# Kernel tuning notes

Hardware: AMD Instinct MI355X
Metric: run time of the kernel (lower is better)

The kernel has to match this reference:

```python
import jax, jax.numpy as jnp
import numpy as np

D = 512
H = 8
DH = D // H
EPS = 1e-5


def _layernorm(x, g, b):
    mu = jnp.mean(x, axis=-1, keepdims=True)
    var = jnp.mean((x - mu) ** 2, axis=-1, keepdims=True)
    return (x - mu) * jax.lax.rsqrt(var + EPS) * g + b


def setup_inputs() -> dict:
    key = jax.random.key(0)
    ks = jax.random.split(key, 10)
    B, S = 4, 2048
    s = 1.0 / np.sqrt(D)
    return {
        "x": jax.random.normal(ks[0], (B, S, D), dtype=jnp.float32),
        "Wq": jax.random.normal(ks[1], (D, D), dtype=jnp.float32) * s,
        "Wk": jax.random.normal(ks[2], (D, D), dtype=jnp.float32) * s,
        "Wv": jax.random.normal(ks[3], (D, D), dtype=jnp.float32) * s,
        "Wo": jax.random.normal(ks[4], (D, D), dtype=jnp.float32) * s,
        "W1": jax.random.normal(ks[5], (4 * D, D), dtype=jnp.float32) * s,
        "b1": jnp.zeros((4 * D,), dtype=jnp.float32),
        "W2": jax.random.normal(ks[6], (D, 4 * D), dtype=jnp.float32) * (1.0 / np.sqrt(4 * D)),
        "b2": jnp.zeros((D,), dtype=jnp.float32),
        "g1": jnp.ones((D,), dtype=jnp.float32),
        "bb1": jnp.zeros((D,), dtype=jnp.float32),
        "g2": jnp.ones((D,), dtype=jnp.float32),
        "bb2": jnp.zeros((D,), dtype=jnp.float32),
    }


def reference(x, Wq, Wk, Wv, Wo, W1, b1, W2, b2, g1, bb1, g2, bb2):
    B, S, _ = x.shape
    # projections (torch Linear: y = x @ W.T), split heads: chunk(-1) == reshape to [B,S,H,DH]
    q = (x @ Wq.T).reshape(B, S, H, DH).transpose(0, 2, 1, 3)  # [B,H,S,DH]
    k = (x @ Wk.T).reshape(B, S, H, DH).transpose(0, 2, 1, 3)
    v = (x @ Wv.T).reshape(B, S, H, DH).transpose(0, 2, 1, 3)
    scores = jnp.einsum("bhsd,bhtd->bhst", q, k) / np.sqrt(DH)  # [B,H,S,S]
    attn = jax.nn.softmax(scores, axis=-1)
    ctx = jnp.einsum("bhst,bhtd->bhsd", attn, v)  # [B,H,S,DH]
    ctx = ctx.transpose(0, 2, 1, 3).reshape(B, S, D)
    h = _layernorm(x + ctx @ Wo.T, g1, bb1)
    mlp = jax.nn.relu(h @ W1.T + b1) @ W2.T + b2
    return _layernorm(h + mlp, g2, bb2)
```

## Files before the change

### kernel.cpp

```cpp
#include <hip/hip_runtime.h>
#include <hip/hip_bf16.h>
#include <cstdint>
#include <cstddef>

typedef short bf16x8 __attribute__((ext_vector_type(8)));
typedef float floatx4 __attribute__((ext_vector_type(4)));
typedef unsigned int uintx4 __attribute__((ext_vector_type(4)));
typedef unsigned short u16;

constexpr int B = 4, S = 2048, D = 512, H = 8, DH = 64;
constexpr int M_ROWS = B * S;
constexpr int D4 = 4 * D;
constexpr float QSCALE = 0.18033688011112042f;

__device__ __forceinline__ u16 f2b(float f) {
  unsigned u = __builtin_bit_cast(unsigned, f);
  u += 0x7fff + ((u >> 16) & 1);
  return (u16)(u >> 16);
}

__device__ __forceinline__ bf16x8 ldfrag(const u16* p) {
  return *reinterpret_cast<const bf16x8*>(p);
}

__device__ __forceinline__ floatx4 mfma16(bf16x8 a, bf16x8 b, floatx4 c) {
  return __builtin_amdgcn_mfma_f32_16x16x32_bf16(a, b, c, 0, 0, 0);
}

__device__ __forceinline__ ushort4 f2b4(float4 v) {
  ushort4 r;
  r.x = f2b(v.x); r.y = f2b(v.y); r.z = f2b(v.z); r.w = f2b(v.w);
  return r;
}

__device__ __forceinline__ void gld16(const u16* g, u16* l) {
  __builtin_amdgcn_global_load_lds(
      (const __attribute__((address_space(1))) void*)g,
      (__attribute__((address_space(3))) void*)l, 16, 0, 0);
}

__global__ void cast_all_kernel(const float4* __restrict__ x,
                                const float4* __restrict__ w1, const float4* __restrict__ w2,
                                const float4* __restrict__ wq, const float4* __restrict__ wk,
                                const float4* __restrict__ wv, const float4* __restrict__ wo,
                                ushort4* __restrict__ xb,
                                ushort4* __restrict__ w1b, ushort4* __restrict__ w2b,
                                ushort4* __restrict__ wqb, ushort4* __restrict__ wkb,
                                ushort4* __restrict__ wvb, ushort4* __restrict__ wob) {
  int i = blockIdx.x * blockDim.x + threadIdx.x;
  constexpr int NX = (M_ROWS * D) / 4;
  constexpr int N1 = (D4 * D) / 4;
  constexpr int NS = (D * D) / 4;
  if (i < NX) { xb[i] = f2b4(x[i]); return; }
  i -= NX;
  if (i < N1) { w1b[i] = f2b4(w1[i]); return; }
  i -= N1;
  if (i < N1) { w2b[i] = f2b4(w2[i]); return; }
  i -= N1;
  const int sel = i >> 16, off = i & (NS - 1);
  const float4* src = sel == 0 ? wq : sel == 1 ? wk : sel == 2 ? wv : wo;
  ushort4* dst = sel == 0 ? wqb : sel == 1 ? wkb : sel == 2 ? wvb : wob;
  dst[off] = f2b4(src[off]);
}

template <int EPI>
__global__ __launch_bounds__(256) void gemm_bt(
    const u16* __restrict__ A, const u16* __restrict__ W,
    const float* __restrict__ bias, void* __restrict__ out0, void* __restrict__ out1,
    int M, int N, int K, int klen) {
  __shared__ __align__(16) u16 As[2][128 * 32];
  __shared__ __align__(16) u16 Bs[2][128 * 32];
  const int wave = threadIdx.x >> 6, lane = threadIdx.x & 63;
  const int quad = lane >> 4, l16 = lane & 15;
  const int rowB = blockIdx.y * 128, colB = blockIdx.x * 128;
  const int rowW = (wave >> 1) * 64, colW = (wave & 1) * 64;
  const int koff = blockIdx.z * klen;
  void* out = blockIdx.z ? out1 : out0;

  floatx4 acc[4][4];
#pragma unroll
  for (int i = 0; i < 4; i++)
#pragma unroll
    for (int j = 0; j < 4; j++) acc[i][j] = (floatx4){0.f,0.f,0.f,0.f};

  const u16* gA = A + (size_t)(rowB + wave * 32 + (lane >> 2)) * K + koff + (lane & 3) * 8;
  const u16* gB = W + (size_t)(colB + wave * 32 + (lane >> 2)) * K + koff + (lane & 3) * 8;
  const int lds_off = wave * 1024;

#pragma unroll
  for (int rr = 0; rr < 2; rr++) {
    gld16(gA + (size_t)rr * 16 * K, &As[0][lds_off + rr * 512]);
    gld16(gB + (size_t)rr * 16 * K, &Bs[0][lds_off + rr * 512]);
  }

  int buf = 0;
  for (int kc = 0; kc < klen; kc += 32, buf ^= 1) {
    __syncthreads();

    if (kc + 32 < klen) {
#pragma unroll
      for (int rr = 0; rr < 2; rr++) {
        gld16(gA + (size_t)rr * 16 * K + kc + 32, &As[buf ^ 1][lds_off + rr * 512]);
        gld16(gB + (size_t)rr * 16 * K + kc + 32, &Bs[buf ^ 1][lds_off + rr * 512]);
      }
    }

    bf16x8 a[4], b[4];
#pragma unroll
    for (int i = 0; i < 4; i++)
      a[i] = ldfrag(&As[buf][(rowW + i * 16 + l16) * 32 + quad * 8]);
#pragma unroll
    for (int j = 0; j < 4; j++)
      b[j] = ldfrag(&Bs[buf][(colW + j * 16 + l16) * 32 + quad * 8]);
#pragma unroll
    for (int i = 0; i < 4; i++)
#pragma unroll
      for (int j = 0; j < 4; j++) acc[i][j] = mfma16(a[i], b[j], acc[i][j]);
  }

#pragma unroll
  for (int i = 0; i < 4; i++) {
#pragma unroll
    for (int j = 0; j < 4; j++) {
      const int gn = colB + colW + j * 16 + l16;
      const float bv = (EPI == 1) ? bias[gn] : 0.f;
#pragma unroll
      for (int r = 0; r < 4; r++) {
        const int gm = rowB + rowW + i * 16 + quad * 4 + r;
        float v = acc[i][j][r] + bv;
        if (EPI == 0) {
          ((float*)out)[(size_t)gm * N + gn] = v;
        } else {
          v = v > 0.f ? v : 0.f;
          ((u16*)out)[(size_t)gm * N + gn] = f2b(v);
        }
      }
    }
  }
}

__global__ __launch_bounds__(256) void qkv_gemm(
    const u16* __restrict__ xb,
    const u16* __restrict__ wq, const u16* __restrict__ wk, const u16* __restrict__ wv,
    u16* __restrict__ q, u16* __restrict__ k, u16* __restrict__ vT) {
  __shared__ __align__(16) u16 As[2][128 * 32];
  __shared__ __align__(16) u16 Bs[2][128 * 32];
  const int which = blockIdx.z;
  const u16* __restrict__ W = which == 0 ? wq : (which == 1 ? wk : wv);
  const int wave = threadIdx.x >> 6, lane = threadIdx.x & 63;
  const int quad = lane >> 4, l16 = lane & 15;
  const int rowB = blockIdx.y * 128, colB = blockIdx.x * 128;
  const int rowW = (wave >> 1) * 64, colW = (wave & 1) * 64;

  floatx4 acc[4][4];
#pragma unroll
  for (int i = 0; i < 4; i++)
#pragma unroll
    for (int j = 0; j < 4; j++) acc[i][j] = (floatx4){0.f,0.f,0.f,0.f};

  const u16* gA = xb + (size_t)(rowB + wave * 32 + (lane >> 2)) * D + (lane & 3) * 8;
  const u16* gB = W + (size_t)(colB + wave * 32 + (lane >> 2)) * D + (lane & 3) * 8;
  const int lds_off = wave * 1024;

#pragma unroll
  for (int rr = 0; rr < 2; rr++) {
    gld16(gA + (size_t)rr * 16 * D, &As[0][lds_off + rr * 512]);
    gld16(gB + (size_t)rr * 16 * D, &Bs[0][lds_off + rr * 512]);
  }

  int buf = 0;
  for (int kc = 0; kc < D; kc += 32, buf ^= 1) {
    __syncthreads();

    if (kc + 32 < D) {
#pragma unroll
      for (int rr = 0; rr < 2; rr++) {
        gld16(gA + (size_t)rr * 16 * D + kc + 32, &As[buf ^ 1][lds_off + rr * 512]);
        gld16(gB + (size_t)rr * 16 * D + kc + 32, &Bs[buf ^ 1][lds_off + rr * 512]);
      }
    }

    bf16x8 a[4], b[4];
#pragma unroll
    for (int i = 0; i < 4; i++)
      a[i] = ldfrag(&As[buf][(rowW + i * 16 + l16) * 32 + quad * 8]);
#pragma unroll
    for (int j = 0; j < 4; j++)
      b[j] = ldfrag(&Bs[buf][(colW + j * 16 + l16) * 32 + quad * 8]);
#pragma unroll
    for (int i = 0; i < 4; i++)
#pragma unroll
      for (int j = 0; j < 4; j++) acc[i][j] = mfma16(a[i], b[j], acc[i][j]);
  }

  const float oscale = (which == 0) ? QSCALE : 1.0f;
  u16* dst01 = which == 0 ? q : k;
#pragma unroll
  for (int i = 0; i < 4; i++) {
#pragma unroll
    for (int j = 0; j < 4; j++) {
      const int gn = colB + colW + j * 16 + l16;
      const int h = gn >> 6, dh = gn & 63;
#pragma unroll
      for (int r = 0; r < 4; r++) {
        const int gm = rowB + rowW + i * 16 + quad * 4 + r;
        const int bb = gm >> 11, s = gm & 2047;
        const u16 val = f2b(acc[i][j][r] * oscale);
        if (which < 2) {
          dst01[((((size_t)bb * H + h) * S) + s) * DH + dh] = val;
        } else {
          const int sl = s & 63;
          const int sw = (s & ~63) | (sl & 35) | ((sl & 12) << 1) | ((sl & 16) >> 2);
          vT[((((size_t)bb * H + h) * DH) + dh) * S + sw] = val;
        }
      }
    }
  }
}

__global__ __launch_bounds__(512, 1) void attn_kernel(
    const u16* __restrict__ q, const u16* __restrict__ k,
    const u16* __restrict__ vT, u16* __restrict__ ctxb) {
  __shared__ __align__(16) u16 kvlds[2][2][2][2][64 * 32];
  __shared__ __align__(16) float ltb[2][4][64];
  const int wave = threadIdx.x >> 6, lane = threadIdx.x & 63;
  const int quad = lane >> 4, l16 = lane & 15;
  const int pair = wave >> 1, khalf = wave & 1;
  const int blk = (blockIdx.x & 7) * 32 + (blockIdx.x >> 3);
  const int w = blk * 4 + pair;
  const int bh = w >> 5, qt = w & 31;
  const int bb = bh >> 3, h = bh & 7;

  const u16* qp = q + ((size_t)bh * S + qt * 64 + l16) * DH + quad * 8;
  bf16x8 qf[4][2];
#pragma unroll
  for (int t = 0; t < 4; t++) {
    qf[t][0] = ldfrag(qp + (size_t)t * 16 * DH);
    qf[t][1] = ldfrag(qp + (size_t)t * 16 * DH + 32);
  }

  const int st = pair * 64 + lane;
  const int srow = st >> 2, sp = (st & 3) * 8;
  const u16* kS = k + (size_t)bh * S * DH + (size_t)(khalf * 1024 + srow) * DH + sp;
  const u16* vS = vT + (size_t)bh * DH * S + (size_t)srow * S + khalf * 1024 + sp;

  floatx4 o[4][4];
#pragma unroll
  for (int t = 0; t < 4; t++)
#pragma unroll
    for (int c = 0; c < 4; c++) o[t][c] = (floatx4){0.f,0.f,0.f,0.f};
  float lacc[4] = {0.f, 0.f, 0.f, 0.f};

  gld16(kS, &kvlds[0][khalf][0][0][pair * 512]);
  gld16(kS + 32, &kvlds[0][khalf][0][1][pair * 512]);
  gld16(vS, &kvlds[0][khalf][1][0][pair * 512]);
  gld16(vS + 32, &kvlds[0][khalf][1][1][pair * 512]);

  int buf = 0;
  for (int kt = 0; kt < S / 2; kt += 64, buf ^= 1) {
    __syncthreads();

    bf16x8 kf[8], vf[8];
#pragma unroll
    for (int i = 0; i < 4; i++) {
      kf[2 * i]     = ldfrag(&kvlds[buf][khalf][0][0][(i * 16 + l16) * 32 + quad * 8]);
      kf[2 * i + 1] = ldfrag(&kvlds[buf][khalf][0][1][(i * 16 + l16) * 32 + quad * 8]);
      vf[2 * i]     = ldfrag(&kvlds[buf][khalf][1][0][(i * 16 + l16) * 32 + quad * 8]);
      vf[2 * i + 1] = ldfrag(&kvlds[buf][khalf][1][1][(i * 16 + l16) * 32 + quad * 8]);
    }

    if (kt + 64 < S / 2) {
      const int nb = buf ^ 1;
      gld16(kS + (size_t)(kt + 64) * DH, &kvlds[nb][khalf][0][0][pair * 512]);
      gld16(kS + (size_t)(kt + 64) * DH + 32, &kvlds[nb][khalf][0][1][pair * 512]);
      gld16(vS + kt + 64, &kvlds[nb][khalf][1][0][pair * 512]);
      gld16(vS + kt + 96, &kvlds[nb][khalf][1][1][pair * 512]);
    }

#pragma unroll
    for (int t = 0; t < 4; t++) {
      floatx4 sc[4];
      __builtin_amdgcn_s_setprio(1);
#pragma unroll
      for (int i = 0; i < 4; i++) {
        floatx4 z = (floatx4){0.f,0.f,0.f,0.f};
        z = mfma16(kf[2 * i], qf[t][0], z);
        z = mfma16(kf[2 * i + 1], qf[t][1], z);
        sc[i] = z;
      }
      __builtin_amdgcn_s_setprio(0);

      unsigned wd[8];
      float a = 0.f;
#pragma unroll
      for (int i = 0; i < 4; i++) {
        const float p0 = __builtin_amdgcn_exp2f(sc[i][0]);
        const float p1 = __builtin_amdgcn_exp2f(sc[i][1]);
        const float p2 = __builtin_amdgcn_exp2f(sc[i][2]);
        const float p3 = __builtin_amdgcn_exp2f(sc[i][3]);
        a += (p0 + p1) + (p2 + p3);
        wd[2 * i] = __builtin_amdgcn_perm(
            __builtin_bit_cast(unsigned, p1) + 0x8000u,
            __builtin_bit_cast(unsigned, p0) + 0x8000u, 0x07060302u);
        wd[2 * i + 1] = __builtin_amdgcn_perm(
            __builtin_bit_cast(unsigned, p3) + 0x8000u,
            __builtin_bit_cast(unsigned, p2) + 0x8000u, 0x07060302u);
      }
      lacc[t] += a;
      const uintx4 lo4 = (uintx4){wd[0], wd[1], wd[2], wd[3]};
      const uintx4 hi4 = (uintx4){wd[4], wd[5], wd[6], wd[7]};
      const bf16x8 pa0 = __builtin_bit_cast(bf16x8, lo4);
      const bf16x8 pa1 = __builtin_bit_cast(bf16x8, hi4);

      __builtin_amdgcn_s_setprio(1);
#pragma unroll
      for (int c = 0; c < 4; c++) {
        o[t][c] = mfma16(pa0, vf[2 * c], o[t][c]);
        o[t][c] = mfma16(pa1, vf[2 * c + 1], o[t][c]);
      }
      __builtin_amdgcn_s_setprio(0);
    }
  }

  float lt[4];
#pragma unroll
  for (int t = 0; t < 4; t++) {
    float l = lacc[t];
    l += __shfl_xor(l, 16);
    l += __shfl_xor(l, 32);
    lt[t] = l;
  }

  __syncthreads();
  float* ob = reinterpret_cast<float*>(&kvlds[0][0][0][0][0]) + pair * 4096;
  if (quad == 0) {
#pragma unroll
    for (int t = 0; t < 4; t++) ltb[khalf][pair][t * 16 + l16] = lt[t];
  }
  if (khalf == 1) {
#pragma unroll
    for (int t = 0; t < 4; t++)
#pragma unroll
      for (int c = 0; c < 4; c++) {
        const int idx = 4 * t + c;
        const int slot = (idx & 8) | ((idx ^ (lane & 7)) & 7);
        *reinterpret_cast<floatx4*>(&ob[lane * 64 + slot * 4]) = o[t][c];
      }
  }
  __syncthreads();
  if (khalf == 0) {
    float inv[4][4];
#pragma unroll
    for (int t = 0; t < 4; t++)
#pragma unroll
      for (int r = 0; r < 4; r++)
        inv[t][r] = 1.0f / (ltb[0][pair][t * 16 + quad * 4 + r] +
                            ltb[1][pair][t * 16 + quad * 4 + r]);

    const size_t crow_base = ((size_t)bb * S) * D + h * DH;
#pragma unroll
    for (int t = 0; t < 4; t++)
#pragma unroll
      for (int c = 0; c < 4; c++) {
        const int idx = 4 * t + c;
        const int slot = (idx & 8) | ((idx ^ (lane & 7)) & 7);
        const floatx4 oo = o[t][c] +
            *reinterpret_cast<const floatx4*>(&ob[lane * 64 + slot * 4]);
        const int dh = c * 16 + l16;
#pragma unroll
        for (int r = 0; r < 4; r++) {
          const int s = qt * 64 + t * 16 + quad * 4 + r;
          ctxb[crow_base + (size_t)s * D + dh] = f2b(oo[r] * inv[t][r]);
        }
      }
  }
}

template <int MODE>
__global__ __launch_bounds__(256) void ln_kernel(
    const void* __restrict__ resid, const float* __restrict__ ya,
    const float* __restrict__ yb, const float* __restrict__ pb,
    const float* __restrict__ g, const float* __restrict__ bvec,
    float* __restrict__ outF, u16* __restrict__ outB) {
  const int wave = threadIdx.x >> 6, lane = threadIdx.x & 63;
  const int row = blockIdx.x * 4 + wave;
  const float* ap = ya + (size_t)row * D + lane * 8;
  const float* bp = yb + (size_t)row * D + lane * 8;
  float v[8];
  const float4 a0 = *(const float4*)ap, a1 = *(const float4*)(ap + 4);
  const float4 b0 = *(const float4*)bp, b1 = *(const float4*)(bp + 4);
  v[0] = a0.x + b0.x; v[1] = a0.y + b0.y; v[2] = a0.z + b0.z; v[3] = a0.w + b0.w;
  v[4] = a1.x + b1.x; v[5] = a1.y + b1.y; v[6] = a1.z + b1.z; v[7] = a1.w + b1.w;
  if (MODE == 0) {
    const float* rp = (const float*)resid + (size_t)row * D + lane * 8;
    const float4 r0 = *(const float4*)rp, r1 = *(const float4*)(rp + 4);
    v[0] += r0.x; v[1] += r0.y; v[2] += r0.z; v[3] += r0.w;
    v[4] += r1.x; v[5] += r1.y; v[6] += r1.z; v[7] += r1.w;
  } else {
    const u16* rp = (const u16*)resid + (size_t)row * D + lane * 8;
    const ushort4 h0 = *(const ushort4*)rp, h1 = *(const ushort4*)(rp + 4);
    v[0] += __builtin_bit_cast(float, (unsigned)h0.x << 16);
    v[1] += __builtin_bit_cast(float, (unsigned)h0.y << 16);
    v[2] += __builtin_bit_cast(float, (unsigned)h0.z << 16);
    v[3] += __builtin_bit_cast(float, (unsigned)h0.w << 16);
    v[4] += __builtin_bit_cast(float, (unsigned)h1.x << 16);
    v[5] += __builtin_bit_cast(float, (unsigned)h1.y << 16);
    v[6] += __builtin_bit_cast(float, (unsigned)h1.z << 16);
    v[7] += __builtin_bit_cast(float, (unsigned)h1.w << 16);
    const float4 p0 = *(const float4*)(pb + lane * 8);
    const float4 p1 = *(const float4*)(pb + lane * 8 + 4);
    v[0] += p0.x; v[1] += p0.y; v[2] += p0.z; v[3] += p0.w;
    v[4] += p1.x; v[5] += p1.y; v[6] += p1.z; v[7] += p1.w;
  }
  float sum = 0.f;
#pragma unroll
  for (int i = 0; i < 8; i++) sum += v[i];
#pragma unroll
  for (int d = 1; d < 64; d <<= 1) sum += __shfl_xor(sum, d);
  const float mu = sum * (1.f / D);
  float vs = 0.f;
#pragma unroll
  for (int i = 0; i < 8; i++) { const float t = v[i] - mu; vs += t * t; }
#pragma unroll
  for (int d = 1; d < 64; d <<= 1) vs += __shfl_xor(vs, d);
  const float rstd = rsqrtf(vs * (1.f / D) + 1e-5f);
#pragma unroll
  for (int i = 0; i < 8; i++) {
    const int col = lane * 8 + i;
    const float o = (v[i] - mu) * rstd * g[col] + bvec[col];
    if (MODE == 0) outB[(size_t)row * D + col] = f2b(o);
    else           outF[(size_t)row * D + col] = o;
  }
}

constexpr size_t OFF_XB  = 0;
constexpr size_t OFF_WQB = 8u << 20;
constexpr size_t OFF_WKB = OFF_WQB + (512u << 10);
constexpr size_t OFF_WVB = OFF_WKB + (512u << 10);
constexpr size_t OFF_WOB = OFF_WVB + (512u << 10);
constexpr size_t OFF_W1B = 10u << 20;
constexpr size_t OFF_W2B = 12u << 20;
constexpr size_t OFF_Q   = 14u << 20;
constexpr size_t OFF_K   = 22u << 20;
constexpr size_t OFF_VT  = 30u << 20;
constexpr size_t OFF_CTX = 38u << 20;
constexpr size_t OFF_Y   = 46u << 20;
constexpr size_t OFF_HB  = 78u << 20;
constexpr size_t OFF_M1B = 86u << 20;

extern "C" void kernel_launch(void* const* d_in, const int* in_sizes, int n_in,
                              void* d_out, int out_size, void* d_ws, size_t ws_size,
                              hipStream_t stream) {
  const float* x  = (const float*)d_in[0];
  const float* Wq = (const float*)d_in[1];
  const float* Wk = (const float*)d_in[2];
  const float* Wv = (const float*)d_in[3];
  const float* Wo = (const float*)d_in[4];
  const float* W1 = (const float*)d_in[5];
  const float* b1 = (const float*)d_in[6];
  const float* W2 = (const float*)d_in[7];
  const float* b2 = (const float*)d_in[8];
  const float* g1 = (const float*)d_in[9];
  const float* bb1 = (const float*)d_in[10];
  const float* g2 = (const float*)d_in[11];
  const float* bb2 = (const float*)d_in[12];

  char* ws = (char*)d_ws;
  u16* xb  = (u16*)(ws + OFF_XB);
  u16* wqb = (u16*)(ws + OFF_WQB);
  u16* wkb = (u16*)(ws + OFF_WKB);
  u16* wvb = (u16*)(ws + OFF_WVB);
  u16* wob = (u16*)(ws + OFF_WOB);
  u16* w1b = (u16*)(ws + OFF_W1B);
  u16* w2b = (u16*)(ws + OFF_W2B);
  u16* qb  = (u16*)(ws + OFF_Q);
  u16* kb  = (u16*)(ws + OFF_K);
  u16* vtb = (u16*)(ws + OFF_VT);
  u16* ctxb = (u16*)(ws + OFF_CTX);
  float* y0 = (float*)(ws + OFF_Y);
  float* y1 = (float*)(ws + OFF_Q);
  u16* hb  = (u16*)(ws + OFF_HB);
  u16* m1b = (u16*)(ws + OFF_M1B);

  {
    const int n4 = (M_ROWS * D) / 4 + (D4 * D) / 4 * 2 + (D * D) / 4 * 4;
    cast_all_kernel<<<(n4 + 255) / 256, 256, 0, stream>>>(
        (const float4*)x, (const float4*)W1, (const float4*)W2, (const float4*)Wq,
        (const float4*)Wk, (const float4*)Wv, (const float4*)Wo,
        (ushort4*)xb, (ushort4*)w1b, (ushort4*)w2b, (ushort4*)wqb,
        (ushort4*)wkb, (ushort4*)wvb, (ushort4*)wob);
  }

  qkv_gemm<<<dim3(D / 128, M_ROWS / 128, 3), 256, 0, stream>>>(xb, wqb, wkb, wvb, qb, kb, vtb);

  attn_kernel<<<B * H * S / 64 / 4, 512, 0, stream>>>(qb, kb, vtb, ctxb);

  gemm_bt<0><<<dim3(D / 128, M_ROWS / 128, 2), 256, 0, stream>>>(
      ctxb, wob, nullptr, y0, y1, M_ROWS, D, D, D / 2);

  ln_kernel<0><<<M_ROWS / 4, 256, 0, stream>>>(
      x, y0, y1, nullptr, g1, bb1, nullptr, hb);

  gemm_bt<1><<<dim3(D4 / 128, M_ROWS / 128, 1), 256, 0, stream>>>(
      hb, w1b, b1, m1b, nullptr, M_ROWS, D4, D, D);

  gemm_bt<0><<<dim3(D / 128, M_ROWS / 128, 2), 256, 0, stream>>>(
      m1b, w2b, nullptr, y0, y1, M_ROWS, D, D4, D4 / 2);

  ln_kernel<1><<<M_ROWS / 4, 256, 0, stream>>>(
      hb, y0, y1, b2, g2, bb2, (float*)d_out, nullptr);
}
```

Measured before the change: 257.3 us.

## Load attention K/V fragments directly from global memory into registers with prefetch

The attention kernel stops staging K and V tiles through double-buffered LDS with block barriers. Each wave now loads its MFMA fragments straight from global memory into registers, alternating between two K register sets so the next tile loads while the current one is computed. Blocks shrink from 512 to 256 threads with two blocks per CU, and the grid doubles. This removes the per-tile __syncthreads and LDS traffic, but loses cross-wave sharing of K/V loads, raises register pressure, and adds exposed global latency on the V loads.

```diff
diff --git a/kernel.cpp b/kernel.cpp
--- a/kernel.cpp
+++ b/kernel.cpp
@@ -218,16 +218,80 @@
   }
 }
 
-__global__ __launch_bounds__(512, 1) void attn_kernel(
+__device__ __forceinline__ void attn_load_k(const u16* kb, int kt, bf16x8 (&kf)[8]) {
+#pragma unroll
+  for (int i = 0; i < 4; i++) {
+    kf[2 * i]     = ldfrag(kb + (size_t)(kt + i * 16) * DH);
+    kf[2 * i + 1] = ldfrag(kb + (size_t)(kt + i * 16) * DH + 32);
+  }
+}
+
+__device__ __forceinline__ void attn_load_v(const u16* vb, int kt, bf16x8 (&vf)[8]) {
+#pragma unroll
+  for (int i = 0; i < 4; i++) {
+    vf[2 * i]     = ldfrag(vb + (size_t)(i * 16) * S + kt);
+    vf[2 * i + 1] = ldfrag(vb + (size_t)(i * 16) * S + kt + 32);
+  }
+}
+
+__device__ __forceinline__ void attn_tile(
+    const bf16x8 (&kf)[8], const bf16x8 (&vf)[8], const bf16x8 (&qf)[4][2],
+    floatx4 (&o)[4][4], float (&lacc)[4]) {
+#pragma unroll
+  for (int t = 0; t < 4; t++) {
+    floatx4 sc[4];
+    __builtin_amdgcn_s_setprio(1);
+#pragma unroll
+    for (int i = 0; i < 4; i++) {
+      floatx4 z = (floatx4){0.f, 0.f, 0.f, 0.f};
+      z = mfma16(kf[2 * i], qf[t][0], z);
+      z = mfma16(kf[2 * i + 1], qf[t][1], z);
+      sc[i] = z;
+    }
+    __builtin_amdgcn_s_setprio(0);
+
+    unsigned wd[8];
+    float a = 0.f;
+#pragma unroll
+    for (int i = 0; i < 4; i++) {
+      const float p0 = __builtin_amdgcn_exp2f(sc[i][0]);
+      const float p1 = __builtin_amdgcn_exp2f(sc[i][1]);
+      const float p2 = __builtin_amdgcn_exp2f(sc[i][2]);
+      const float p3 = __builtin_amdgcn_exp2f(sc[i][3]);
+      a += (p0 + p1) + (p2 + p3);
+      wd[2 * i] = __builtin_amdgcn_perm(
+          __builtin_bit_cast(unsigned, p1) + 0x8000u,
+          __builtin_bit_cast(unsigned, p0) + 0x8000u, 0x07060302u);
+      wd[2 * i + 1] = __builtin_amdgcn_perm(
+          __builtin_bit_cast(unsigned, p3) + 0x8000u,
+          __builtin_bit_cast(unsigned, p2) + 0x8000u, 0x07060302u);
+    }
+    lacc[t] += a;
+    const uintx4 lo4 = (uintx4){wd[0], wd[1], wd[2], wd[3]};
+    const uintx4 hi4 = (uintx4){wd[4], wd[5], wd[6], wd[7]};
+    const bf16x8 pa0 = __builtin_bit_cast(bf16x8, lo4);
+    const bf16x8 pa1 = __builtin_bit_cast(bf16x8, hi4);
+
+    __builtin_amdgcn_s_setprio(1);
+#pragma unroll
+    for (int c = 0; c < 4; c++) {
+      o[t][c] = mfma16(pa0, vf[2 * c], o[t][c]);
+      o[t][c] = mfma16(pa1, vf[2 * c + 1], o[t][c]);
+    }
+    __builtin_amdgcn_s_setprio(0);
+  }
+}
+
+__global__ __launch_bounds__(256, 2) void attn_kernel(
     const u16* __restrict__ q, const u16* __restrict__ k,
     const u16* __restrict__ vT, u16* __restrict__ ctxb) {
-  __shared__ __align__(16) u16 kvlds[2][2][2][2][64 * 32];
-  __shared__ __align__(16) float ltb[2][4][64];
+  __shared__ __align__(16) float obuf[2][64 * 64];
+  __shared__ float ltb[2][2][64];
   const int wave = threadIdx.x >> 6, lane = threadIdx.x & 63;
   const int quad = lane >> 4, l16 = lane & 15;
   const int pair = wave >> 1, khalf = wave & 1;
-  const int blk = (blockIdx.x & 7) * 32 + (blockIdx.x >> 3);
-  const int w = blk * 4 + pair;
+  const int blk = (blockIdx.x & 7) * 64 + (blockIdx.x >> 3);
+  const int w = blk * 2 + pair;
   const int bh = w >> 5, qt = w & 31;
   const int bb = bh >> 3, h = bh & 7;
 
@@ -239,87 +303,25 @@
     qf[t][1] = ldfrag(qp + (size_t)t * 16 * DH + 32);
   }
 
-  const int st = pair * 64 + lane;
-  const int srow = st >> 2, sp = (st & 3) * 8;
-  const u16* kS = k + (size_t)bh * S * DH + (size_t)(khalf * 1024 + srow) * DH + sp;
-  const u16* vS = vT + (size_t)bh * DH * S + (size_t)srow * S + khalf * 1024 + sp;
+  const u16* kb = k + ((size_t)bh * S + khalf * 1024 + l16) * DH + quad * 8;
+  const u16* vb = vT + ((size_t)bh * DH + l16) * S + khalf * 1024 + quad * 8;
 
   floatx4 o[4][4];
 #pragma unroll
   for (int t = 0; t < 4; t++)
 #pragma unroll
-    for (int c = 0; c < 4; c++) o[t][c] = (floatx4){0.f,0.f,0.f,0.f};
+    for (int c = 0; c < 4; c++) o[t][c] = (floatx4){0.f, 0.f, 0.f, 0.f};
   float lacc[4] = {0.f, 0.f, 0.f, 0.f};
 
-  gld16(kS, &kvlds[0][khalf][0][0][pair * 512]);
-  gld16(kS + 32, &kvlds[0][khalf][0][1][pair * 512]);
-  gld16(vS, &kvlds[0][khalf][1][0][pair * 512]);
-  gld16(vS + 32, &kvlds[0][khalf][1][1][pair * 512]);
-
-  int buf = 0;
-  for (int kt = 0; kt < S / 2; kt += 64, buf ^= 1) {
-    __syncthreads();
-
-    bf16x8 kf[8], vf[8];
-#pragma unroll
-    for (int i = 0; i < 4; i++) {
-      kf[2 * i]     = ldfrag(&kvlds[buf][khalf][0][0][(i * 16 + l16) * 32 + quad * 8]);
-      kf[2 * i + 1] = ldfrag(&kvlds[buf][khalf][0][1][(i * 16 + l16) * 32 + quad * 8]);
-      vf[2 * i]     = ldfrag(&kvlds[buf][khalf][1][0][(i * 16 + l16) * 32 + quad * 8]);
-      vf[2 * i + 1] = ldfrag(&kvlds[buf][khalf][1][1][(i * 16 + l16) * 32 + quad * 8]);
-    }
-
-    if (kt + 64 < S / 2) {
-      const int nb = buf ^ 1;
-      gld16(kS + (size_t)(kt + 64) * DH, &kvlds[nb][khalf][0][0][pair * 512]);
-      gld16(kS + (size_t)(kt + 64) * DH + 32, &kvlds[nb][khalf][0][1][pair * 512]);
-      gld16(vS + kt + 64, &kvlds[nb][khalf][1][0][pair * 512]);
-      gld16(vS + kt + 96, &kvlds[nb][khalf][1][1][pair * 512]);
-    }
-
-#pragma unroll
-    for (int t = 0; t < 4; t++) {
-      floatx4 sc[4];
-      __builtin_amdgcn_s_setprio(1);
-#pragma unroll
-      for (int i = 0; i < 4; i++) {
-        floatx4 z = (floatx4){0.f,0.f,0.f,0.f};
-        z = mfma16(kf[2 * i], qf[t][0], z);
-        z = mfma16(kf[2 * i + 1], qf[t][1], z);
-        sc[i] = z;
-      }
-      __builtin_amdgcn_s_setprio(0);
-
-      unsigned wd[8];
-      float a = 0.f;
-#pragma unroll
-      for (int i = 0; i < 4; i++) {
-        const float p0 = __builtin_amdgcn_exp2f(sc[i][0]);
-        const float p1 = __builtin_amdgcn_exp2f(sc[i][1]);
-        const float p2 = __builtin_amdgcn_exp2f(sc[i][2]);
-        const float p3 = __builtin_amdgcn_exp2f(sc[i][3]);
-        a += (p0 + p1) + (p2 + p3);
-        wd[2 * i] = __builtin_amdgcn_perm(
-            __builtin_bit_cast(unsigned, p1) + 0x8000u,
-            __builtin_bit_cast(unsigned, p0) + 0x8000u, 0x07060302u);
-        wd[2 * i + 1] = __builtin_amdgcn_perm(
-            __builtin_bit_cast(unsigned, p3) + 0x8000u,
-            __builtin_bit_cast(unsigned, p2) + 0x8000u, 0x07060302u);
-      }
-      lacc[t] += a;
-      const uintx4 lo4 = (uintx4){wd[0], wd[1], wd[2], wd[3]};
-      const uintx4 hi4 = (uintx4){wd[4], wd[5], wd[6], wd[7]};
-      const bf16x8 pa0 = __builtin_bit_cast(bf16x8, lo4);
-      const bf16x8 pa1 = __builtin_bit_cast(bf16x8, hi4);
-
-      __builtin_amdgcn_s_setprio(1);
-#pragma unroll
-      for (int c = 0; c < 4; c++) {
-        o[t][c] = mfma16(pa0, vf[2 * c], o[t][c]);
-        o[t][c] = mfma16(pa1, vf[2 * c + 1], o[t][c]);
-      }
-      __builtin_amdgcn_s_setprio(0);
-    }
+  bf16x8 kfA[8], kfB[8], vf[8];
+  attn_load_k(kb, 0, kfA);
+  for (int kt = 0; kt < S / 2; kt += 128) {
+    attn_load_v(vb, kt, vf);
+    attn_load_k(kb, kt + 64, kfB);
+    attn_tile(kfA, vf, qf, o, lacc);
+    attn_load_v(vb, kt + 64, vf);
+    if (kt + 128 < S / 2) attn_load_k(kb, kt + 128, kfA);
+    attn_tile(kfB, vf, qf, o, lacc);
   }
 
   float lt[4];
@@ -331,8 +333,7 @@
     lt[t] = l;
   }
 
-  __syncthreads();
-  float* ob = reinterpret_cast<float*>(&kvlds[0][0][0][0][0]) + pair * 4096;
+  float* ob = obuf[pair];
   if (quad == 0) {
 #pragma unroll
     for (int t = 0; t < 4; t++) ltb[khalf][pair][t * 16 + l16] = lt[t];
@@ -493,7 +494,7 @@
 
   qkv_gemm<<<dim3(D / 128, M_ROWS / 128, 3), 256, 0, stream>>>(xb, wqb, wkb, wvb, qb, kb, vtb);
 
-  attn_kernel<<<B * H * S / 64 / 4, 512, 0, stream>>>(qb, kb, vtb, ctxb);
+  attn_kernel<<<B * H * S / 64 / 2, 256, 0, stream>>>(qb, kb, vtb, ctxb);
 
   gemm_bt<0><<<dim3(D / 128, M_ROWS / 128, 2), 256, 0, stream>>>(
       ctxb, wob, nullptr, y0, y1, M_ROWS, D, D, D / 2);
```

Result: slower. 349.6 us (+35.9%).

## Triple-buffer K/V tiles in attention with explicit vmcnt waits

Applied to the files above, without the earlier changes.

Replaces the double-buffered K/V shared-memory staging with a three-slot ring that prefetches two tiles ahead. Each iteration uses a partial vmcnt wait plus a raw barrier instead of __syncthreads, so global loads for later tiles can stay in flight while the current tile is computed. It also drops the s_setprio hints around the MFMA blocks. The cost is 50% more LDS for the K/V staging, and the hand-written vmcnt counts must match the compiler's load ordering exactly.

```diff
diff --git a/kernel.cpp b/kernel.cpp
--- a/kernel.cpp
+++ b/kernel.cpp
@@ -221,7 +221,7 @@
 __global__ __launch_bounds__(512, 1) void attn_kernel(
     const u16* __restrict__ q, const u16* __restrict__ k,
     const u16* __restrict__ vT, u16* __restrict__ ctxb) {
-  __shared__ __align__(16) u16 kvlds[2][2][2][2][64 * 32];
+  __shared__ __align__(16) u16 kvbuf[3][2][2][2][64 * 32];
   __shared__ __align__(16) float ltb[2][4][64];
   const int wave = threadIdx.x >> 6, lane = threadIdx.x & 63;
   const int quad = lane >> 4, l16 = lane & 15;
@@ -251,36 +251,44 @@
     for (int c = 0; c < 4; c++) o[t][c] = (floatx4){0.f,0.f,0.f,0.f};
   float lacc[4] = {0.f, 0.f, 0.f, 0.f};
 
-  gld16(kS, &kvlds[0][khalf][0][0][pair * 512]);
-  gld16(kS + 32, &kvlds[0][khalf][0][1][pair * 512]);
-  gld16(vS, &kvlds[0][khalf][1][0][pair * 512]);
-  gld16(vS + 32, &kvlds[0][khalf][1][1][pair * 512]);
-
-  int buf = 0;
-  for (int kt = 0; kt < S / 2; kt += 64, buf ^= 1) {
-    __syncthreads();
+#pragma unroll
+  for (int T = 0; T < 2; T++) {
+    gld16(kS + (size_t)T * 64 * DH,      &kvbuf[T][khalf][0][0][pair * 512]);
+    gld16(kS + (size_t)T * 64 * DH + 32, &kvbuf[T][khalf][0][1][pair * 512]);
+    gld16(vS + T * 64,                   &kvbuf[T][khalf][1][0][pair * 512]);
+    gld16(vS + T * 64 + 32,              &kvbuf[T][khalf][1][1][pair * 512]);
+  }
+
+  int rb = 0, wb = 2;
+  for (int it = 0; it < 16; ++it) {
+    if (it < 15) asm volatile("s_waitcnt vmcnt(4)" ::: "memory");
+    else         asm volatile("s_waitcnt vmcnt(0)" ::: "memory");
+    __builtin_amdgcn_s_barrier();
+    __builtin_amdgcn_sched_barrier(0);
+
+    if (it + 2 < 16) {
+      gld16(kS + (size_t)(it + 2) * 64 * DH,      &kvbuf[wb][khalf][0][0][pair * 512]);
+      gld16(kS + (size_t)(it + 2) * 64 * DH + 32, &kvbuf[wb][khalf][0][1][pair * 512]);
+      gld16(vS + (it + 2) * 64,                   &kvbuf[wb][khalf][1][0][pair * 512]);
+      gld16(vS + (it + 2) * 64 + 32,              &kvbuf[wb][khalf][1][1][pair * 512]);
+    }
 
     bf16x8 kf[8], vf[8];
+    const u16* kb0 = &kvbuf[rb][khalf][0][0][0];
+    const u16* kb1 = &kvbuf[rb][khalf][0][1][0];
+    const u16* vb0 = &kvbuf[rb][khalf][1][0][0];
+    const u16* vb1 = &kvbuf[rb][khalf][1][1][0];
 #pragma unroll
     for (int i = 0; i < 4; i++) {
-      kf[2 * i]     = ldfrag(&kvlds[buf][khalf][0][0][(i * 16 + l16) * 32 + quad * 8]);
-      kf[2 * i + 1] = ldfrag(&kvlds[buf][khalf][0][1][(i * 16 + l16) * 32 + quad * 8]);
-      vf[2 * i]     = ldfrag(&kvlds[buf][khalf][1][0][(i * 16 + l16) * 32 + quad * 8]);
-      vf[2 * i + 1] = ldfrag(&kvlds[buf][khalf][1][1][(i * 16 + l16) * 32 + quad * 8]);
-    }
-
-    if (kt + 64 < S / 2) {
-      const int nb = buf ^ 1;
-      gld16(kS + (size_t)(kt + 64) * DH, &kvlds[nb][khalf][0][0][pair * 512]);
-      gld16(kS + (size_t)(kt + 64) * DH + 32, &kvlds[nb][khalf][0][1][pair * 512]);
-      gld16(vS + kt + 64, &kvlds[nb][khalf][1][0][pair * 512]);
-      gld16(vS + kt + 96, &kvlds[nb][khalf][1][1][pair * 512]);
+      kf[2 * i]     = ldfrag(&kb0[(i * 16 + l16) * 32 + quad * 8]);
+      kf[2 * i + 1] = ldfrag(&kb1[(i * 16 + l16) * 32 + quad * 8]);
+      vf[2 * i]     = ldfrag(&vb0[(i * 16 + l16) * 32 + quad * 8]);
+      vf[2 * i + 1] = ldfrag(&vb1[(i * 16 + l16) * 32 + quad * 8]);
     }
 
 #pragma unroll
     for (int t = 0; t < 4; t++) {
       floatx4 sc[4];
-      __builtin_amdgcn_s_setprio(1);
 #pragma unroll
       for (int i = 0; i < 4; i++) {
         floatx4 z = (floatx4){0.f,0.f,0.f,0.f};
@@ -288,7 +296,6 @@
         z = mfma16(kf[2 * i + 1], qf[t][1], z);
         sc[i] = z;
       }
-      __builtin_amdgcn_s_setprio(0);
 
       unsigned wd[8];
       float a = 0.f;
@@ -312,14 +319,15 @@
       const bf16x8 pa0 = __builtin_bit_cast(bf16x8, lo4);
       const bf16x8 pa1 = __builtin_bit_cast(bf16x8, hi4);
 
-      __builtin_amdgcn_s_setprio(1);
 #pragma unroll
       for (int c = 0; c < 4; c++) {
         o[t][c] = mfma16(pa0, vf[2 * c], o[t][c]);
         o[t][c] = mfma16(pa1, vf[2 * c + 1], o[t][c]);
       }
-      __builtin_amdgcn_s_setprio(0);
-    }
+    }
+
+    rb = rb == 2 ? 0 : rb + 1;
+    wb = wb == 2 ? 0 : wb + 1;
   }
 
   float lt[4];
@@ -332,7 +340,7 @@
   }
 
   __syncthreads();
-  float* ob = reinterpret_cast<float*>(&kvlds[0][0][0][0][0]) + pair * 4096;
+  float* ob = reinterpret_cast<float*>(&kvbuf[0][0][0][0][0]) + pair * 4096;
   if (quad == 0) {
 #pragma unroll
     for (int t = 0; t < 4; t++) ltb[khalf][pair][t * 16 + l16] = lt[t];
```

After: 260.3 us. No clear change (+1.2%).
